# Kernel optimization log

Measured on AMD Instinct MI355X. Metric: run time of the kernel, lower is better.

Reference implementation:

```python
import jax, jax.numpy as jnp
import numpy as np

N, C, HI, WI = 8, 3, 512, 512   # src_img NCHW (input_img_size)
HO, WO = 2048, 2048             # output canvas (output_img_size[2:])
EPS = 1e-8


def _transform_one(img, coor_row):
    """Replicates: sigmoid box params -> theta -> F.affine_grid -> F.grid_sample
    (bilinear, zeros padding, align_corners=False). Theta has zero off-diagonals,
    so the grid is separable in x/y and the bilinear sample factorizes.
    img: [C, HI, WI]; coor_row: [4]. Returns (sample [C,HO,WO], mask [HO,WO])."""
    x = jax.nn.sigmoid(coor_row[0]) * WO
    y = jax.nn.sigmoid(coor_row[1]) * HO
    w = jax.nn.sigmoid(coor_row[2]) * WO
    h = jax.nn.sigmoid(coor_row[3]) * HO
    a = WO / (w + EPS)
    tx = 2.0 / WO * (WO / 2.0 - x) * a
    b = HO / (h + EPS)
    ty = 2.0 / HO * (HO / 2.0 - y) * b
    # affine_grid base coords (align_corners=False): center-of-pixel normalized
    xs = (2.0 * jnp.arange(WO, dtype=img.dtype) + 1.0) / WO - 1.0
    ys = (2.0 * jnp.arange(HO, dtype=img.dtype) + 1.0) / HO - 1.0
    gx = a * xs + tx          # [WO]
    gy = b * ys + ty          # [HO]
    # grid_sample unnormalize (align_corners=False)
    ix = ((gx + 1.0) * WI - 1.0) / 2.0
    iy = ((gy + 1.0) * HI - 1.0) / 2.0
    x0f = jnp.floor(ix); y0f = jnp.floor(iy)
    wx1 = ix - x0f; wx0 = 1.0 - wx1
    wy1 = iy - y0f; wy0 = 1.0 - wy1
    x0 = x0f.astype(jnp.int32); x1 = x0 + 1
    y0 = y0f.astype(jnp.int32); y1 = y0 + 1
    vx0 = ((x0 >= 0) & (x0 < WI)).astype(img.dtype)
    vx1 = ((x1 >= 0) & (x1 < WI)).astype(img.dtype)
    vy0 = ((y0 >= 0) & (y0 < HI)).astype(img.dtype)
    vy1 = ((y1 >= 0) & (y1 < HI)).astype(img.dtype)
    x0c = jnp.clip(x0, 0, WI - 1); x1c = jnp.clip(x1, 0, WI - 1)
    y0c = jnp.clip(y0, 0, HI - 1); y1c = jnp.clip(y1, 0, HI - 1)
    wyv0 = wy0 * vy0; wyv1 = wy1 * vy1
    wxv0 = wx0 * vx0; wxv1 = wx1 * vx1
    # separable bilinear gather with zero padding
    rows = img[:, y0c, :] * wyv0[None, :, None] + img[:, y1c, :] * wyv1[None, :, None]  # [C,HO,WI]
    samp = rows[:, :, x0c] * wxv0[None, None, :] + rows[:, :, x1c] * wxv1[None, None, :]  # [C,HO,WO]
    # grid_sample of an all-ones mask == sum of in-bounds bilinear weights (separable)
    mask = (wyv0 + wyv1)[:, None] * (wxv0 + wxv1)[None, :]  # [HO,WO]
    return samp, mask


def _composite(src_img, bg_img, coor):
    def step(bg, inp):
        img, c = inp
        s, m = _transform_one(img, c)
        bg = bg * (1.0 - m)[None, None] + (s * m[None])[None]
        return bg, None
    bg, _ = jax.lax.scan(step, bg_img, (src_img, coor))
    return bg


def setup_inputs() -> dict:
    key = jax.random.key(0)
    k1, k2, k3 = jax.random.split(key, 3)
    src_img = jax.random.normal(k1, (N, C, HI, WI), dtype=jnp.float32)
    bg_img = jax.random.uniform(k2, (1, C, HO, WO), dtype=jnp.float32)
    coor = jax.random.normal(k3, (N, 4), dtype=jnp.float32)  # nn.Parameter
    return {"src_img": src_img, "bg_img": bg_img, "coor": coor}


def reference(src_img, bg_img, coor):
    return _composite(src_img, bg_img, coor)
```

## Files before the change

kernel.cpp:

```cpp
#include <hip/hip_runtime.h>

#define WI 512
#define HI 512
#define WO 2048
#define HO 2048
#define NIMG 8
#define CCH 3
#define EPS 1e-8f
#define ROWS 8

__global__ void diffcomp_params(const float* __restrict__ coor,
                                float4* __restrict__ params) {
    int n = threadIdx.x;
    if (n < NIMG) {
        float cx = coor[n * 4 + 0];
        float cy = coor[n * 4 + 1];
        float cw = coor[n * 4 + 2];
        float ch = coor[n * 4 + 3];
        float x = (1.0f / (1.0f + expf(-cx))) * (float)WO;
        float y = (1.0f / (1.0f + expf(-cy))) * (float)HO;
        float w = (1.0f / (1.0f + expf(-cw))) * (float)WO;
        float h = (1.0f / (1.0f + expf(-ch))) * (float)HO;
        float a  = (float)WO / (w + EPS);
        float tx = (2.0f / (float)WO) * ((float)WO * 0.5f - x) * a;
        float b  = (float)HO / (h + EPS);
        float ty = (2.0f / (float)HO) * ((float)HO * 0.5f - y) * b;
        params[n] = make_float4(a, tx, b, ty);
    }
}

__launch_bounds__(256)
__global__ void diffcomp_main(const float* __restrict__ src,
                              const float* __restrict__ bg,
                              const float4* __restrict__ params,
                              float* __restrict__ out) {
    const int wo  = blockIdx.x * 256 + threadIdx.x;
    const int ho0 = blockIdx.y * ROWS;

    float4 P[NIMG];
#pragma unroll
    for (int n = 0; n < NIMG; n++) P[n] = params[n];

    float wxv0[NIMG], wxv1[NIMG], mx[NIMG];
    int   x0c[NIMG], x1c[NIMG];
    const float xs = (2.0f * (float)wo + 1.0f) / (float)WO - 1.0f;
#pragma unroll
    for (int n = 0; n < NIMG; n++) {
        float a  = P[n].x, tx = P[n].y;
        float gx = a * xs + tx;
        float ix = (((gx + 1.0f) * (float)WI) - 1.0f) * 0.5f;
        float x0f = floorf(ix);
        float wx1 = ix - x0f;
        float wx0 = 1.0f - wx1;
        float x1f = x0f + 1.0f;
        float vx0 = (x0f >= 0.0f && x0f < (float)WI) ? 1.0f : 0.0f;
        float vx1 = (x1f >= 0.0f && x1f < (float)WI) ? 1.0f : 0.0f;
        wxv0[n] = wx0 * vx0;
        wxv1[n] = wx1 * vx1;
        x0c[n] = (int)fminf(fmaxf(x0f, 0.0f), (float)(WI - 1));
        x1c[n] = (int)fminf(fmaxf(x1f, 0.0f), (float)(WI - 1));
        mx[n] = wxv0[n] + wxv1[n];
    }

    for (int r = 0; r < ROWS; r++) {
        const int ho = ho0 + r;
        const float ys = (2.0f * (float)ho + 1.0f) / (float)HO - 1.0f;
        const int pix = ho * WO + wo;

        float acc0 = bg[0 * HO * WO + pix];
        float acc1 = bg[1 * HO * WO + pix];
        float acc2 = bg[2 * HO * WO + pix];

#pragma unroll
        for (int n = 0; n < NIMG; n++) {
            float b  = P[n].z, ty = P[n].w;
            float gy = b * ys + ty;
            float iy = (((gy + 1.0f) * (float)HI) - 1.0f) * 0.5f;
            float y0f = floorf(iy);
            float wy1 = iy - y0f;
            float wy0 = 1.0f - wy1;
            float y1f = y0f + 1.0f;
            float vy0 = (y0f >= 0.0f && y0f < (float)HI) ? 1.0f : 0.0f;
            float vy1 = (y1f >= 0.0f && y1f < (float)HI) ? 1.0f : 0.0f;
            float wyv0 = wy0 * vy0;
            float wyv1 = wy1 * vy1;
            float my = wyv0 + wyv1;
            float m  = my * mx[n];
            if (m > 0.0f) {
                int y0i = (int)fminf(fmaxf(y0f, 0.0f), (float)(HI - 1));
                int y1i = (int)fminf(fmaxf(y1f, 0.0f), (float)(HI - 1));
                const float* ib = src + n * (CCH * HI * WI);
                const int o00 = y0i * WI + x0c[n];
                const int o01 = y0i * WI + x1c[n];
                const int o10 = y1i * WI + x0c[n];
                const int o11 = y1i * WI + x1c[n];
                const float om = 1.0f - m;
                float s0, s1, s2;
                {
                    const float* p = ib + 0 * HI * WI;
                    float v00 = p[o00], v01 = p[o01], v10 = p[o10], v11 = p[o11];
                    s0 = (v00 * wyv0 + v10 * wyv1) * wxv0[n]
                       + (v01 * wyv0 + v11 * wyv1) * wxv1[n];
                }
                {
                    const float* p = ib + 1 * HI * WI;
                    float v00 = p[o00], v01 = p[o01], v10 = p[o10], v11 = p[o11];
                    s1 = (v00 * wyv0 + v10 * wyv1) * wxv0[n]
                       + (v01 * wyv0 + v11 * wyv1) * wxv1[n];
                }
                {
                    const float* p = ib + 2 * HI * WI;
                    float v00 = p[o00], v01 = p[o01], v10 = p[o10], v11 = p[o11];
                    s2 = (v00 * wyv0 + v10 * wyv1) * wxv0[n]
                       + (v01 * wyv0 + v11 * wyv1) * wxv1[n];
                }
                acc0 = acc0 * om + s0 * m;
                acc1 = acc1 * om + s1 * m;
                acc2 = acc2 * om + s2 * m;
            }
        }

        out[0 * HO * WO + pix] = acc0;
        out[1 * HO * WO + pix] = acc1;
        out[2 * HO * WO + pix] = acc2;
    }
}

extern "C" void kernel_launch(void* const* d_in, const int* in_sizes, int n_in,
                              void* d_out, int out_size, void* d_ws, size_t ws_size,
                              hipStream_t stream) {
    const float* src  = (const float*)d_in[0];
    const float* bg   = (const float*)d_in[1];
    const float* coor = (const float*)d_in[2];
    float* out = (float*)d_out;
    float4* params = (float4*)d_ws;

    hipLaunchKernelGGL(diffcomp_params, dim3(1), dim3(64), 0, stream, coor, params);
    dim3 grid(WO / 256, HO / ROWS);
    hipLaunchKernelGGL(diffcomp_main, grid, dim3(256), 0, stream,
                       src, bg, params, out);
}
```

Measured before the change: 154.9 us.

## Fuse param kernel and stage vertically-blended source rows in shared memory per output row

Replaces the two-kernel design with one fused kernel that handles one output row per block and computes box parameters in-block. For each image covering the row, the two source rows are blended vertically into a double-buffered LDS tile, which turns four scattered global gathers per pixel into two LDS reads. Each thread now handles 8 pixels with vectorized bg/out access, and blocks are assigned rows through a scrambled index to balance load. The cost is a __syncthreads per covering image and more per-block work for the param computation.

```diff
diff --git a/kernel.cpp b/kernel.cpp
--- a/kernel.cpp
+++ b/kernel.cpp
@@ -7,122 +7,166 @@
 #define NIMG 8
 #define CCH 3
 #define EPS 1e-8f
-#define ROWS 8
+#define PLANE (HI * WI)
 
-__global__ void diffcomp_params(const float* __restrict__ coor,
-                                float4* __restrict__ params) {
-    int n = threadIdx.x;
-    if (n < NIMG) {
-        float cx = coor[n * 4 + 0];
-        float cy = coor[n * 4 + 1];
-        float cw = coor[n * 4 + 2];
-        float ch = coor[n * 4 + 3];
-        float x = (1.0f / (1.0f + expf(-cx))) * (float)WO;
-        float y = (1.0f / (1.0f + expf(-cy))) * (float)HO;
-        float w = (1.0f / (1.0f + expf(-cw))) * (float)WO;
-        float h = (1.0f / (1.0f + expf(-ch))) * (float)HO;
-        float a  = (float)WO / (w + EPS);
-        float tx = (2.0f / (float)WO) * ((float)WO * 0.5f - x) * a;
-        float b  = (float)HO / (h + EPS);
-        float ty = (2.0f / (float)HO) * ((float)HO * 0.5f - y) * b;
-        params[n] = make_float4(a, tx, b, ty);
+__device__ __forceinline__ void ycalc(const float4 P, const float ys,
+                                      float& wyv0, float& wyv1,
+                                      int& y0o, int& y1o) {
+    const float gy  = P.z * ys + P.w;
+    const float iy  = ((gy + 1.0f) * (float)HI - 1.0f) * 0.5f;
+    const float y0f = floorf(iy);
+    const float fy1 = iy - y0f;
+    const float fy0 = 1.0f - fy1;
+    const float y1f = y0f + 1.0f;
+    const float v0  = (y0f >= 0.0f && y0f < (float)HI) ? 1.0f : 0.0f;
+    const float v1  = (y1f >= 0.0f && y1f < (float)HI) ? 1.0f : 0.0f;
+    wyv0 = fy0 * v0;
+    wyv1 = fy1 * v1;
+    y0o = (int)fminf(fmaxf(y0f, 0.0f), (float)(HI - 1)) * WI;
+    y1o = (int)fminf(fmaxf(y1f, 0.0f), (float)(HI - 1)) * WI;
+}
+
+__device__ __forceinline__ void stage_rows(float (*dst)[WI],
+                                           const float* __restrict__ src,
+                                           const int n,
+                                           const float wyv0, const float wyv1,
+                                           const int y0o, const int y1o,
+                                           const int tid) {
+    if (tid < 128) {
+        const int x = tid << 2;
+        const float* base = src + n * (CCH * PLANE);
+#pragma unroll
+        for (int c = 0; c < CCH; c++) {
+            const float4 r0 = *(const float4*)(base + c * PLANE + y0o + x);
+            const float4 r1 = *(const float4*)(base + c * PLANE + y1o + x);
+            float4 rc;
+            rc.x = r0.x * wyv0 + r1.x * wyv1;
+            rc.y = r0.y * wyv0 + r1.y * wyv1;
+            rc.z = r0.z * wyv0 + r1.z * wyv1;
+            rc.w = r0.w * wyv0 + r1.w * wyv1;
+            *(float4*)&dst[c][x] = rc;
+        }
     }
 }
 
 __launch_bounds__(256)
-__global__ void diffcomp_main(const float* __restrict__ src,
-                              const float* __restrict__ bg,
-                              const float4* __restrict__ params,
-                              float* __restrict__ out) {
-    const int wo  = blockIdx.x * 256 + threadIdx.x;
-    const int ho0 = blockIdx.y * ROWS;
+__global__ void diffcomp_fused(const float* __restrict__ src,
+                               const float* __restrict__ bg,
+                               const float* __restrict__ coor,
+                               float* __restrict__ out) {
+    __shared__ float  cs[2][CCH][WI];
+    __shared__ float4 prm[NIMG];
 
-    float4 P[NIMG];
-#pragma unroll
-    for (int n = 0; n < NIMG; n++) P[n] = params[n];
+    const int tid = threadIdx.x;
+    const int ho  = (int)((blockIdx.x * 997u) & 2047u);
 
-    float wxv0[NIMG], wxv1[NIMG], mx[NIMG];
-    int   x0c[NIMG], x1c[NIMG];
-    const float xs = (2.0f * (float)wo + 1.0f) / (float)WO - 1.0f;
+    if (tid < NIMG) {
+        const float cx = coor[tid * 4 + 0];
+        const float cy = coor[tid * 4 + 1];
+        const float cw = coor[tid * 4 + 2];
+        const float chh = coor[tid * 4 + 3];
+        const float x = (1.0f / (1.0f + expf(-cx))) * (float)WO;
+        const float y = (1.0f / (1.0f + expf(-cy))) * (float)HO;
+        const float w = (1.0f / (1.0f + expf(-cw))) * (float)WO;
+        const float h = (1.0f / (1.0f + expf(-chh))) * (float)HO;
+        const float a  = (float)WO / (w + EPS);
+        const float tx = (2.0f / (float)WO) * ((float)WO * 0.5f - x) * a;
+        const float b  = (float)HO / (h + EPS);
+        const float ty = (2.0f / (float)HO) * ((float)HO * 0.5f - y) * b;
+        prm[tid] = make_float4(a, tx, b, ty);
+    }
+    __syncthreads();
+
+    const float ys = (2.0f * (float)ho + 1.0f) / (float)HO - 1.0f;
+
+    unsigned cov = 0u;
 #pragma unroll
     for (int n = 0; n < NIMG; n++) {
-        float a  = P[n].x, tx = P[n].y;
-        float gx = a * xs + tx;
-        float ix = (((gx + 1.0f) * (float)WI) - 1.0f) * 0.5f;
-        float x0f = floorf(ix);
-        float wx1 = ix - x0f;
-        float wx0 = 1.0f - wx1;
-        float x1f = x0f + 1.0f;
-        float vx0 = (x0f >= 0.0f && x0f < (float)WI) ? 1.0f : 0.0f;
-        float vx1 = (x1f >= 0.0f && x1f < (float)WI) ? 1.0f : 0.0f;
-        wxv0[n] = wx0 * vx0;
-        wxv1[n] = wx1 * vx1;
-        x0c[n] = (int)fminf(fmaxf(x0f, 0.0f), (float)(WI - 1));
-        x1c[n] = (int)fminf(fmaxf(x1f, 0.0f), (float)(WI - 1));
-        mx[n] = wxv0[n] + wxv1[n];
+        float w0, w1; int a0, a1;
+        ycalc(prm[n], ys, w0, w1, a0, a1);
+        if (w0 + w1 > 0.0f) cov |= (1u << n);
     }
 
-    for (int r = 0; r < ROWS; r++) {
-        const int ho = ho0 + r;
-        const float ys = (2.0f * (float)ho + 1.0f) / (float)HO - 1.0f;
-        const int pix = ho * WO + wo;
+    const int rowbase = ho * WO + (tid << 3);
+    float acc[CCH][8];
+#pragma unroll
+    for (int c = 0; c < CCH; c++) {
+        const float4 b0 = *(const float4*)(bg + c * HO * WO + rowbase);
+        const float4 b1 = *(const float4*)(bg + c * HO * WO + rowbase + 4);
+        acc[c][0] = b0.x; acc[c][1] = b0.y; acc[c][2] = b0.z; acc[c][3] = b0.w;
+        acc[c][4] = b1.x; acc[c][5] = b1.y; acc[c][6] = b1.z; acc[c][7] = b1.w;
+    }
 
-        float acc0 = bg[0 * HO * WO + pix];
-        float acc1 = bg[1 * HO * WO + pix];
-        float acc2 = bg[2 * HO * WO + pix];
+    if (cov) {
+        int cur = (int)__builtin_ctz(cov);
+        unsigned rest = cov & (cov - 1u);
+
+        float4 Pc = prm[cur];
+        float w0c, w1c; int y0c, y1c;
+        ycalc(Pc, ys, w0c, w1c, y0c, y1c);
+        float myc = w0c + w1c;
+        stage_rows(cs[0], src, cur, w0c, w1c, y0c, y1c, tid);
+        __syncthreads();
+
+        int s = 0;
+        while (true) {
+            const int nxt = rest ? (int)__builtin_ctz(rest) : -1;
+            float4 Pn; float mynxt = 0.0f;
+            if (nxt >= 0) {
+                Pn = prm[nxt];
+                float w0n, w1n; int a0, a1;
+                ycalc(Pn, ys, w0n, w1n, a0, a1);
+                mynxt = w0n + w1n;
+                stage_rows(cs[s ^ 1], src, nxt, w0n, w1n, a0, a1, tid);
+            }
+
+            const float a  = Pc.x;
+            const float tx = Pc.y;
+#pragma unroll
+            for (int p = 0; p < 8; p++) {
+                const int wo = (tid << 3) + p;
+                const float xs  = (2.0f * (float)wo + 1.0f) / (float)WO - 1.0f;
+                const float gx  = a * xs + tx;
+                const float ix  = ((gx + 1.0f) * (float)WI - 1.0f) * 0.5f;
+                const float x0f = floorf(ix);
+                const float fx1 = ix - x0f;
+                const float fx0 = 1.0f - fx1;
+                const float vx0 = (x0f >= 0.0f && x0f < (float)WI) ? 1.0f : 0.0f;
+                const float vx1 = (x0f >= -1.0f && x0f < (float)(WI - 1)) ? 1.0f : 0.0f;
+                const float wxv0 = fx0 * vx0;
+                const float wxv1 = fx1 * vx1;
+                const int bse = (int)fminf(fmaxf(x0f, 0.0f), (float)(WI - 2));
+                const int x0i = (int)fminf(fmaxf(x0f, 0.0f), (float)(WI - 1));
+                const int x1i = (int)fminf(fmaxf(x0f + 1.0f, 0.0f), (float)(WI - 1));
+                const bool hi0 = (x0i != bse);
+                const bool hi1 = (x1i != bse);
+                const float m  = myc * (wxv0 + wxv1);
+                const float om = 1.0f - m;
+#pragma unroll
+                for (int c = 0; c < CCH; c++) {
+                    const float qa = cs[s][c][bse];
+                    const float qb = cs[s][c][bse + 1];
+                    const float v0 = hi0 ? qb : qa;
+                    const float v1 = hi1 ? qb : qa;
+                    const float sc = v0 * wxv0 + v1 * wxv1;
+                    acc[c][p] = acc[c][p] * om + sc * m;
+                }
+            }
+
+            __syncthreads();
+            if (nxt < 0) break;
+            Pc = Pn; myc = mynxt;
+            rest &= rest - 1u;
+            s ^= 1;
+        }
+    }
 
 #pragma unroll
-        for (int n = 0; n < NIMG; n++) {
-            float b  = P[n].z, ty = P[n].w;
-            float gy = b * ys + ty;
-            float iy = (((gy + 1.0f) * (float)HI) - 1.0f) * 0.5f;
-            float y0f = floorf(iy);
-            float wy1 = iy - y0f;
-            float wy0 = 1.0f - wy1;
-            float y1f = y0f + 1.0f;
-            float vy0 = (y0f >= 0.0f && y0f < (float)HI) ? 1.0f : 0.0f;
-            float vy1 = (y1f >= 0.0f && y1f < (float)HI) ? 1.0f : 0.0f;
-            float wyv0 = wy0 * vy0;
-            float wyv1 = wy1 * vy1;
-            float my = wyv0 + wyv1;
-            float m  = my * mx[n];
-            if (m > 0.0f) {
-                int y0i = (int)fminf(fmaxf(y0f, 0.0f), (float)(HI - 1));
-                int y1i = (int)fminf(fmaxf(y1f, 0.0f), (float)(HI - 1));
-                const float* ib = src + n * (CCH * HI * WI);
-                const int o00 = y0i * WI + x0c[n];
-                const int o01 = y0i * WI + x1c[n];
-                const int o10 = y1i * WI + x0c[n];
-                const int o11 = y1i * WI + x1c[n];
-                const float om = 1.0f - m;
-                float s0, s1, s2;
-                {
-                    const float* p = ib + 0 * HI * WI;
-                    float v00 = p[o00], v01 = p[o01], v10 = p[o10], v11 = p[o11];
-                    s0 = (v00 * wyv0 + v10 * wyv1) * wxv0[n]
-                       + (v01 * wyv0 + v11 * wyv1) * wxv1[n];
-                }
-                {
-                    const float* p = ib + 1 * HI * WI;
-                    float v00 = p[o00], v01 = p[o01], v10 = p[o10], v11 = p[o11];
-                    s1 = (v00 * wyv0 + v10 * wyv1) * wxv0[n]
-                       + (v01 * wyv0 + v11 * wyv1) * wxv1[n];
-                }
-                {
-                    const float* p = ib + 2 * HI * WI;
-                    float v00 = p[o00], v01 = p[o01], v10 = p[o10], v11 = p[o11];
-                    s2 = (v00 * wyv0 + v10 * wyv1) * wxv0[n]
-                       + (v01 * wyv0 + v11 * wyv1) * wxv1[n];
-                }
-                acc0 = acc0 * om + s0 * m;
-                acc1 = acc1 * om + s1 * m;
-                acc2 = acc2 * om + s2 * m;
-            }
-        }
-
-        out[0 * HO * WO + pix] = acc0;
-        out[1 * HO * WO + pix] = acc1;
-        out[2 * HO * WO + pix] = acc2;
+    for (int c = 0; c < CCH; c++) {
+        const float4 o0 = make_float4(acc[c][0], acc[c][1], acc[c][2], acc[c][3]);
+        const float4 o1 = make_float4(acc[c][4], acc[c][5], acc[c][6], acc[c][7]);
+        *(float4*)(out + c * HO * WO + rowbase)     = o0;
+        *(float4*)(out + c * HO * WO + rowbase + 4) = o1;
     }
 }
 
@@ -133,10 +177,8 @@
     const float* bg   = (const float*)d_in[1];
     const float* coor = (const float*)d_in[2];
     float* out = (float*)d_out;
-    float4* params = (float4*)d_ws;
+    (void)d_ws; (void)ws_size;
 
-    hipLaunchKernelGGL(diffcomp_params, dim3(1), dim3(64), 0, stream, coor, params);
-    dim3 grid(WO / 256, HO / ROWS);
-    hipLaunchKernelGGL(diffcomp_main, grid, dim3(256), 0, stream,
-                       src, bg, params, out);
+    hipLaunchKernelGGL(diffcomp_fused, dim3(HO), dim3(256), 0, stream,
+                       src, bg, coor, out);
 }
```

Result: faster. 134.5 us (-13.2%).
